# Kernel optimization log

Hardware: AMD Instinct MI355X
Metric: run time of the kernel (lower is better)

The kernel has to match this reference:

```python
import jax, jax.numpy as jnp
import numpy as np

B, NPG, K = 8, 2048, 20   # graphs, nodes per graph, kNN fanout
N = B * NPG
OUT = 16


def _bn(h, g, b, eps=1e-5):
    # BatchNorm1d (training-mode batch stats, biased var), channels last
    ax = tuple(range(h.ndim - 1))
    m = h.mean(ax)
    v = h.var(ax)
    return g * (h - m) * jax.lax.rsqrt(v + eps) + b


def _mlp(h, w, b, g, be):
    # Sequential(Linear, ReLU, BatchNorm1d)
    return _bn(jax.nn.relu(h @ w + b), g, be)


def _knn(f, k):
    # k nearest (squared euclidean), self included like torch_cluster.knn(x, x)
    sq = jnp.sum(f * f, axis=-1)
    d = sq[:, None] - 2.0 * (f @ f.T) + sq[None, :]   # [n, n]
    return jax.lax.top_k(-d, k)[1]                    # [n, k]


def setup_inputs() -> dict:
    key = jax.random.key(0)
    ks = jax.random.split(key, 16)

    def w(i, shape):
        return jax.random.normal(ks[i], shape, jnp.float32) * (1.0 / np.sqrt(shape[0]))

    return {
        "pos": jax.random.normal(ks[0], (N, 3), jnp.float32),
        "x": jax.random.normal(ks[1], (N, 1), jnp.float32),
        "batch": jnp.repeat(jnp.arange(B, dtype=jnp.int32), NPG),  # equal-size graphs
        # conv1 edge MLP: Linear(8,64)+ReLU+BN
        "w1": w(2, (8, 64)), "b1": jnp.zeros((64,), jnp.float32), "g1": jnp.ones((64,), jnp.float32), "be1": jnp.zeros((64,), jnp.float32),
        # conv2 edge MLP: Linear(128,128)+ReLU+BN
        "w2": w(3, (128, 128)), "b2": jnp.zeros((128,), jnp.float32), "g2": jnp.ones((128,), jnp.float32), "be2": jnp.zeros((128,), jnp.float32),
        # fc: Linear(192,256)+ReLU+BN
        "wf": w(4, (192, 256)), "bf": jnp.zeros((256,), jnp.float32), "gf": jnp.ones((256,), jnp.float32), "bef": jnp.zeros((256,), jnp.float32),
        # out head: Linear(256,128)+ReLU+BN, Linear(128,64)+ReLU+BN, Linear(64,OUT)
        "wo1": w(5, (256, 128)), "bo1": jnp.zeros((128,), jnp.float32), "go1": jnp.ones((128,), jnp.float32), "beo1": jnp.zeros((128,), jnp.float32),
        "wo2": w(6, (128, 64)), "bo2": jnp.zeros((64,), jnp.float32), "go2": jnp.ones((64,), jnp.float32), "beo2": jnp.zeros((64,), jnp.float32),
        "wo3": w(7, (64, OUT)), "bo3": jnp.zeros((OUT,), jnp.float32),
    }


def reference(pos, x, batch, w1, b1, g1, be1, w2, b2, g2, be2,
              wf, bf, gf, bef, wo1, bo1, go1, beo1, wo2, bo2, go2, beo2, wo3, bo3):
    # ---- conv1: DynamicEdgeConv over ALL nodes (called without batch) ----
    f0 = jnp.concatenate([pos, x], axis=-1)            # [N, 4]
    idx1 = _knn(f0, K)                                 # [N, K] global kNN
    xi = f0[:, None, :]                                # [N, 1, 4]
    xj = jnp.take(f0, idx1, axis=0)                    # [N, K, 4]
    e1 = jnp.concatenate([jnp.broadcast_to(xi, xj.shape), xj - xi], axis=-1)  # [N,K,8]
    x1 = _mlp(e1, w1, b1, g1, be1).max(axis=1)         # max aggr -> [N, 64]

    # ---- conv2: DynamicEdgeConv with per-graph kNN (equal-size graphs) ----
    x1b = x1.reshape(B, NPG, -1)                       # [B, n, 64]
    idx2 = jax.vmap(lambda f: _knn(f, K))(x1b)         # [B, n, K] local indices
    xj2 = jax.vmap(lambda f, i: f[i])(x1b, idx2)       # [B, n, K, 64]
    xi2 = x1b[:, :, None, :]
    e2 = jnp.concatenate([jnp.broadcast_to(xi2, xj2.shape), xj2 - xi2], axis=-1)
    e2 = e2.reshape(N, K, 128)                         # BN over all edges jointly
    x2 = _mlp(e2, w2, b2, g2, be2).max(axis=1)         # [N, 128]

    # ---- fc + global max pool + head ----
    h = _mlp(jnp.concatenate([x1, x2], axis=-1), wf, bf, gf, bef)  # [N, 256]
    hp = h.reshape(B, NPG, -1).max(axis=1)             # global_max_pool -> [B, 256]
    hp = _mlp(hp, wo1, bo1, go1, beo1)                 # Dropout(0.5) = identity (eval)
    hp = _mlp(hp, wo2, bo2, go2, beo2)
    logits = hp @ wo3 + bo3                            # [B, OUT]
    return jax.nn.log_softmax(logits, axis=1)
```

## Files before the change

### kernel.cpp

```cpp
#include <hip/hip_runtime.h>
#include <math.h>

#define NPTS 16384
#define KNB 20
#define SCAP 512

typedef __attribute__((ext_vector_type(8))) short short8;
typedef __attribute__((ext_vector_type(4))) float f32x4;

static const size_t OFF_F0   = 0;
static const size_t OFF_SSQ0 = OFF_F0   + (size_t)NPTS*4*4;
static const size_t OFF_IDX1 = OFF_SSQ0 + (size_t)NPTS*4;
static const size_t OFF_XMX1 = OFF_IDX1 + (size_t)NPTS*KNB*4;
static const size_t OFF_XMN1 = OFF_XMX1 + (size_t)NPTS*64*4;
static const size_t OFF_SUM1 = OFF_XMN1 + (size_t)NPTS*64*4;
static const size_t OFF_X1   = OFF_SUM1 + 512;
static const size_t OFF_SSQ1 = OFF_X1   + (size_t)NPTS*64*4;
static const size_t OFF_IDX2 = OFF_SSQ1 + (size_t)NPTS*4;
static const size_t OFF_XMX2 = OFF_IDX2 + (size_t)NPTS*KNB*4;
static const size_t OFF_XMN2 = OFF_XMX2 + (size_t)NPTS*128*4;
static const size_t OFF_SUM2 = OFF_XMN2 + (size_t)NPTS*128*4;
static const size_t OFF_X2   = OFF_SUM2 + 1024;
static const size_t OFF_SUMF = OFF_X2   + (size_t)NPTS*128*4;
static const size_t OFF_HPMX = OFF_SUMF + 2048;
static const size_t OFF_HPMN = OFF_HPMX + 8*256*4;

__device__ __forceinline__ float dot4f(float4 a, float4 b) {
  return a.x*b.x + a.y*b.y + a.z*b.z + a.w*b.w;
}

__device__ __forceinline__ float dot64v(const float* a, const float4* b4) {
  float s = 0.f;
  #pragma unroll
  for (int d4 = 0; d4 < 16; ++d4) {
    float4 b = b4[d4];
    s += a[4*d4+0]*b.x + a[4*d4+1]*b.y + a[4*d4+2]*b.z + a[4*d4+3]*b.w;
  }
  return s;
}

__device__ __forceinline__ short f2bf(float x) {
  union { float f; unsigned u; } v; v.f = x;
  unsigned r = (v.u + 0x7FFFu + ((v.u >> 16) & 1u)) >> 16;
  return (short)r;
}

__device__ __forceinline__ void ce(float& a, int& ai, float& b, int& bi) {
  bool sw = b < a;
  float d0 = sw ? b : a;  float d1 = sw ? a : b;
  int   j0 = sw ? bi : ai; int  j1 = sw ? ai : bi;
  a = d0; ai = j0; b = d1; bi = j1;
}

__device__ __forceinline__ void sort16(float (&d)[16], int (&ix)[16]) {
  #pragma unroll
  for (int k = 2; k <= 16; k <<= 1) {
    #pragma unroll
    for (int j = k >> 1; j > 0; j >>= 1) {
      #pragma unroll
      for (int i = 0; i < 16; ++i) {
        int l = i ^ j;
        if (l > i) {
          if ((i & k) == 0) ce(d[i], ix[i], d[l], ix[l]);
          else              ce(d[l], ix[l], d[i], ix[i]);
        }
      }
    }
  }
}

__device__ __forceinline__ void bimerge32(float (&rd)[32], int (&ri)[32]) {
  #pragma unroll
  for (int j = 16; j > 0; j >>= 1) {
    #pragma unroll
    for (int i = 0; i < 32; ++i) {
      int l = i ^ j;
      if (l > i) ce(rd[i], ri[i], rd[l], ri[l]);
    }
  }
}

__device__ __forceinline__ void merge16(float (&rd)[32], int (&ri)[32],
                                        float (&bd)[16], int (&bi)[16]) {
  #pragma unroll
  for (int k = 0; k < 16; ++k) {
    bool sw = bd[15-k] < rd[16+k];
    rd[16+k] = sw ? bd[15-k] : rd[16+k];
    ri[16+k] = sw ? bi[15-k] : ri[16+k];
  }
  bimerge32(rd, ri);
}

__device__ __forceinline__ void mergelane(float (&rd)[32], int (&ri)[32], int mask) {
  float pd[32]; int pi[32];
  #pragma unroll
  for (int s = 0; s < 32; ++s) { pd[s] = __shfl_xor(rd[s], mask); pi[s] = __shfl_xor(ri[s], mask); }
  #pragma unroll
  for (int k = 0; k < 32; ++k) {
    bool sw = pd[31-k] < rd[k];
    rd[k] = sw ? pd[31-k] : rd[k];
    ri[k] = sw ? pi[31-k] : ri[k];
  }
  bimerge32(rd, ri);
}

__device__ __forceinline__ void vce(float& a, float& b) {
  float lo = fminf(a, b);
  b = fmaxf(a, b);
  a = lo;
}

__device__ __forceinline__ void vsort16(float (&d)[16]) {
  #pragma unroll
  for (int k = 2; k <= 16; k <<= 1) {
    #pragma unroll
    for (int j = k >> 1; j > 0; j >>= 1) {
      #pragma unroll
      for (int i = 0; i < 16; ++i) {
        int l = i ^ j;
        if (l > i) {
          if ((i & k) == 0) vce(d[i], d[l]);
          else              vce(d[l], d[i]);
        }
      }
    }
  }
}

__device__ __forceinline__ void vbimerge32(float (&rd)[32]) {
  #pragma unroll
  for (int j = 16; j > 0; j >>= 1) {
    #pragma unroll
    for (int i = 0; i < 32; ++i) {
      int l = i ^ j;
      if (l > i) vce(rd[i], rd[l]);
    }
  }
}

__device__ __forceinline__ void vmerge16(float (&rd)[32], float (&bd)[16]) {
  #pragma unroll
  for (int k = 0; k < 16; ++k) rd[16+k] = fminf(rd[16+k], bd[15-k]);
  vbimerge32(rd);
}

__device__ __forceinline__ void vmergelane(float (&rd)[32], int mask) {
  float pd[32];
  #pragma unroll
  for (int s = 0; s < 32; ++s) pd[s] = __shfl_xor(rd[s], mask);
  #pragma unroll
  for (int k = 0; k < 32; ++k) rd[k] = fminf(rd[k], pd[31-k]);
  vbimerge32(rd);
}

__global__ __launch_bounds__(256) void k_init(const float* __restrict__ pos, const float* __restrict__ x,
                                              const float* __restrict__ w2,
                                              float4* __restrict__ f0, float* __restrict__ ssq,
                                              short* __restrict__ wtg,
                                              float* sum1, float* sum2, float* sumF,
                                              unsigned* hpmx, unsigned* hpmn) {
  int gt = blockIdx.x*256 + threadIdx.x;
  float4 f;
  f.x = pos[3*gt+0]; f.y = pos[3*gt+1]; f.z = pos[3*gt+2]; f.w = x[gt];
  f0[gt] = f;
  ssq[gt] = dot4f(f, f);
  { int c = gt >> 7, k = gt & 127; wtg[c*128 + k] = f2bf(w2[k*128 + c]); }
  if (gt < 128) sum1[gt] = 0.f;
  if (gt < 256) sum2[gt] = 0.f;
  if (gt < 512) sumF[gt] = 0.f;
  if (gt < 2048) { hpmx[gt] = 0u; hpmn[gt] = 0x7f800000u; }
}

__global__ __launch_bounds__(256) void k_knn1(const float4* __restrict__ f0, const float* __restrict__ ssq,
                                              int* __restrict__ idx1) {
  __shared__ int survj[8][SCAP];
  __shared__ int scnt[8];
  __shared__ float rowT[8];
  int t = threadIdx.x;
  int r = t >> 5;
  int lane = t & 31;
  int row = blockIdx.x*8 + r;
  if (t < 8) scnt[t] = 0;
  float4 fi = f0[row];
  float sqi = ssq[row];
  {
    float rd[32];
    #pragma unroll
    for (int s = 0; s < 32; ++s) rd[s] = INFINITY;
    #pragma unroll
    for (int b = 0; b < 4; ++b) {
      float bd[16];
      #pragma unroll
      for (int u = 0; u < 16; ++u) {
        int j = b*512 + u*32 + lane;
        float4 c = f0[j];
        bd[u] = (sqi - 2.f*dot4f(fi, c)) + ssq[j];
      }
      vsort16(bd);
      vmerge16(rd, bd);
    }
    vmergelane(rd, 1); vmergelane(rd, 2); vmergelane(rd, 4);
    vmergelane(rd, 8); vmergelane(rd, 16);
    if (lane == 0) rowT[r] = rd[19];
  }
  __syncthreads();
  {
    float4 fr[8]; float sr[8], Tr[8];
    #pragma unroll
    for (int q = 0; q < 8; ++q) {
      fr[q] = f0[blockIdx.x*8 + q];
      sr[q] = ssq[blockIdx.x*8 + q];
      Tr[q] = rowT[q];
    }
    #pragma unroll 4
    for (int k = 0; k < 64; ++k) {
      int j = k*256 + t;
      float4 c = f0[j];
      float cq = ssq[j];
      #pragma unroll
      for (int q = 0; q < 8; ++q) {
        float d = (sr[q] - 2.f*dot4f(fr[q], c)) + cq;
        if (d <= Tr[q]) {
          int slot = atomicAdd(&scnt[q], 1);
          if (slot < SCAP) survj[q][slot] = j;
        }
      }
    }
  }
  __syncthreads();
  int n = scnt[r] < SCAP ? scnt[r] : SCAP;
  float rd[32]; int ri[32];
  #pragma unroll
  for (int s = 0; s < 32; ++s) { rd[s] = INFINITY; ri[s] = 0; }
  {
    float bd[16]; int bix[16];
    #pragma unroll
    for (int u = 0; u < 16; ++u) {
      int s = u*32 + lane;
      if (s < n) {
        int j = survj[r][s];
        float4 c = f0[j];
        bd[u] = (sqi - 2.f*dot4f(fi, c)) + ssq[j];
        bix[u] = j;
      } else { bd[u] = INFINITY; bix[u] = 0; }
    }
    sort16(bd, bix);
    merge16(rd, ri, bd, bix);
  }
  mergelane(rd, ri, 1); mergelane(rd, ri, 2); mergelane(rd, ri, 4);
  mergelane(rd, ri, 8); mergelane(rd, ri, 16);
  if (lane == 0) {
    int4* p = (int4*)&idx1[row*KNB];
    p[0] = make_int4(ri[0],ri[1],ri[2],ri[3]);
    p[1] = make_int4(ri[4],ri[5],ri[6],ri[7]);
    p[2] = make_int4(ri[8],ri[9],ri[10],ri[11]);
    p[3] = make_int4(ri[12],ri[13],ri[14],ri[15]);
    p[4] = make_int4(ri[16],ri[17],ri[18],ri[19]);
  }
}

__global__ __launch_bounds__(256) void k_mlp1(const float4* __restrict__ f0, const int* __restrict__ idx1,
                                              const float* __restrict__ w1, const float* __restrict__ b1,
                                              float* __restrict__ xmx, float* __restrict__ xmn,
                                              float* __restrict__ sums) {
  __shared__ float rs[256], rs2[256];
  int t = threadIdx.x;
  int c = t & 63;
  int w = t >> 6;
  float wc[8];
  #pragma unroll
  for (int d = 0; d < 8; ++d) wc[d] = w1[d*64 + c];
  float bc = b1[c];
  float s = 0.f, s2 = 0.f;
  for (int p = 0; p < 8; ++p) {
    int i = blockIdx.x*32 + p*4 + w;
    float4 fi = f0[i];
    float mx = -INFINITY, mn = INFINITY;
    #pragma unroll
    for (int k = 0; k < KNB; ++k) {
      int j = idx1[i*KNB + k];
      float4 fj = f0[j];
      float h = bc + fi.x*wc[0] + fi.y*wc[1] + fi.z*wc[2] + fi.w*wc[3]
                   + (fj.x-fi.x)*wc[4] + (fj.y-fi.y)*wc[5] + (fj.z-fi.z)*wc[6] + (fj.w-fi.w)*wc[7];
      h = fmaxf(h, 0.f);
      mx = fmaxf(mx, h); mn = fminf(mn, h);
      s += h; s2 += h*h;
    }
    xmx[i*64+c] = mx; xmn[i*64+c] = mn;
  }
  rs[t] = s; rs2[t] = s2;
  __syncthreads();
  if (t < 64) {
    atomicAdd(&sums[c],      rs[t]+rs[t+64]+rs[t+128]+rs[t+192]);
    atomicAdd(&sums[64+c],   rs2[t]+rs2[t+64]+rs2[t+128]+rs2[t+192]);
  }
}

__global__ __launch_bounds__(256) void k_bn1apply(const float* __restrict__ sums, const float* __restrict__ g,
                                                  const float* __restrict__ be, const float* __restrict__ xmx,
                                                  const float* __restrict__ xmn, float* __restrict__ x1) {
  __shared__ float sc_s[64], sh_s[64];
  int t = threadIdx.x;
  if (t < 64) {
    float m = sums[t] * (1.f/327680.f);
    float v = sums[64+t] * (1.f/327680.f) - m*m;
    float sc = g[t] / sqrtf(v + 1e-5f);
    sc_s[t] = sc; sh_s[t] = be[t] - m*sc;
  }
  __syncthreads();
  int c = t & 63;
  int i = blockIdx.x*4 + (t>>6);
  float sc = sc_s[c], sh = sh_s[c];
  float val = (sc >= 0.f) ? xmx[i*64+c] : xmn[i*64+c];
  x1[i*64+c] = sc*val + sh;
}

__global__ __launch_bounds__(256) void k_ssq1(const float* __restrict__ x1, float* __restrict__ ssq1) {
  int i = blockIdx.x*256 + threadIdx.x;
  alignas(16) float f[64];
  #pragma unroll
  for (int d4 = 0; d4 < 16; ++d4) ((float4*)f)[d4] = ((const float4*)x1)[i*16 + d4];
  ssq1[i] = dot64v(f, (const float4*)f);
}

__global__ __launch_bounds__(256) void k_knn2(const float* __restrict__ x1, const float* __restrict__ ssq1,
                                              int* __restrict__ idx2) {
  __shared__ __align__(16) float tf[128][68];
  __shared__ float tq[128];
  int t = threadIdx.x;
  int row = blockIdx.x*32 + (t>>3);
  int lane = t & 7;
  int cbase = (row >> 11) << 11;
  alignas(16) float fi[64];
  #pragma unroll
  for (int d4 = 0; d4 < 16; ++d4) ((float4*)fi)[d4] = ((const float4*)x1)[row*16 + d4];
  float sqi = ssq1[row];
  float rd[32]; int ri[32];
  #pragma unroll
  for (int s = 0; s < 32; ++s) { rd[s] = INFINITY; ri[s] = 0; }
  for (int tile = 0; tile < 16; ++tile) {
    int base = cbase + tile*128;
    __syncthreads();
    for (int v = t; v < 128*16; v += 256) {
      int jl = v >> 4, d4 = v & 15;
      *(float4*)&tf[jl][d4*4] = ((const float4*)x1)[(base+jl)*16 + d4];
    }
    if (t < 128) tq[t] = ssq1[base + t];
    __syncthreads();
    float bd[16]; int bix[16];
    #pragma unroll
    for (int u = 0; u < 16; ++u) {
      int jl = u*8 + lane;
      bd[u] = (sqi - 2.f*dot64v(fi, (const float4*)&tf[jl][0])) + tq[jl];
      bix[u] = base + jl;
    }
    sort16(bd, bix);
    merge16(rd, ri, bd, bix);
  }
  mergelane(rd, ri, 1);
  mergelane(rd, ri, 2);
  mergelane(rd, ri, 4);
  if (lane == 0) {
    int4* p = (int4*)&idx2[row*KNB];
    p[0] = make_int4(ri[0],ri[1],ri[2],ri[3]);
    p[1] = make_int4(ri[4],ri[5],ri[6],ri[7]);
    p[2] = make_int4(ri[8],ri[9],ri[10],ri[11]);
    p[3] = make_int4(ri[12],ri[13],ri[14],ri[15]);
    p[4] = make_int4(ri[16],ri[17],ri[18],ri[19]);
  }
}

__global__ __launch_bounds__(256) void k_mlp2(const float* __restrict__ x1, const int* __restrict__ idx2,
                                              const short* __restrict__ wtg, const float* __restrict__ w2,
                                              const float* __restrict__ b2,
                                              float* __restrict__ xmx, float* __restrict__ xmn,
                                              float* __restrict__ sums) {
  __shared__ __align__(16) short Elds[4*32*72];
  __shared__ float xi_s[4][64];
  __shared__ float vi[4][128];
  __shared__ int js[4][KNB];
  int t = threadIdx.x;
  if (t < 4*KNB) js[t/KNB][t%KNB] = idx2[blockIdx.x*4*KNB + t];
  {
    int p = t >> 6, k = t & 63;
    xi_s[p][k] = x1[(blockIdx.x*4 + p)*64 + k];
  }
  __syncthreads();
  #pragma unroll
  for (int v2 = 0; v2 < 2; ++v2) {
    int v = t + v2*256;
    int p = v >> 7, c = v & 127;
    float a = b2[c];
    #pragma unroll 8
    for (int k = 0; k < 64; ++k) a += xi_s[p][k] * w2[k*128 + c];
    vi[p][c] = a;
  }
  #pragma unroll
  for (int cc = 0; cc < 4; ++cc) {
    int v = t + cc*256;
    int p  = v >> 8;
    int rr = (v >> 3) & 31;
    int kc = v & 7;
    short8 outv = {0,0,0,0,0,0,0,0};
    if (rr < KNB) {
      int j = js[p][rr];
      float4 j0 = ((const float4*)x1)[j*16 + kc*2];
      float4 j1 = ((const float4*)x1)[j*16 + kc*2 + 1];
      const float* xp = &xi_s[p][kc*8];
      outv[0]=f2bf(j0.x-xp[0]); outv[1]=f2bf(j0.y-xp[1]); outv[2]=f2bf(j0.z-xp[2]); outv[3]=f2bf(j0.w-xp[3]);
      outv[4]=f2bf(j1.x-xp[4]); outv[5]=f2bf(j1.y-xp[5]); outv[6]=f2bf(j1.z-xp[6]); outv[7]=f2bf(j1.w-xp[7]);
    }
    *(short8*)&Elds[p*2304 + rr*72 + kc*8] = outv;
  }
  __syncthreads();
  int w = t >> 6, l = t & 63;
  int colA = w*32 + (l & 15);
  int colB = colA + 16;
  short8 bfr[2][2];
  #pragma unroll
  for (int n = 0; n < 2; ++n)
    #pragma unroll
    for (int kb = 0; kb < 2; ++kb) {
      int col = w*32 + n*16 + (l & 15);
      int k0 = 64 + kb*32 + (l >> 4)*8;
      bfr[n][kb] = *(const short8*)&wtg[col*128 + k0];
    }
  float sT0=0.f, qT0=0.f, sT1=0.f, qT1=0.f;
  #pragma unroll
  for (int p = 0; p < 4; ++p) {
    int i = blockIdx.x*4 + p;
    float vA = vi[p][colA], vB = vi[p][colB];
    float mx0=-INFINITY, mn0=INFINITY, s0=0.f, q0=0.f;
    float mx1=-INFINITY, mn1=INFINITY, s1=0.f, q1=0.f;
    #pragma unroll
    for (int m = 0; m < 2; ++m) {
      short8 af[2];
      #pragma unroll
      for (int kb = 0; kb < 2; ++kb) {
        int row = m*16 + (l & 15);
        int k0 = kb*32 + (l >> 4)*8;
        af[kb] = *(short8*)&Elds[p*2304 + row*72 + k0];
      }
      f32x4 acc0 = {vA, vA, vA, vA};
      f32x4 acc1 = {vB, vB, vB, vB};
      #pragma unroll
      for (int kb = 0; kb < 2; ++kb) {
        acc0 = __builtin_amdgcn_mfma_f32_16x16x32_bf16(af[kb], bfr[0][kb], acc0, 0, 0, 0);
        acc1 = __builtin_amdgcn_mfma_f32_16x16x32_bf16(af[kb], bfr[1][kb], acc1, 0, 0, 0);
      }
      int rbase = (l >> 4)*4 + m*16;
      #pragma unroll
      for (int reg = 0; reg < 4; ++reg) {
        bool valid = (rbase + reg) < KNB;
        float h0 = fmaxf(acc0[reg], 0.f);
        float h1 = fmaxf(acc1[reg], 0.f);
        if (valid) {
          mx0 = fmaxf(mx0, h0); mn0 = fminf(mn0, h0); s0 += h0; q0 += h0*h0;
          mx1 = fmaxf(mx1, h1); mn1 = fminf(mn1, h1); s1 += h1; q1 += h1*h1;
        }
      }
    }
    #pragma unroll
    for (int dlt = 16; dlt <= 32; dlt <<= 1) {
      mx0 = fmaxf(mx0, __shfl_xor(mx0, dlt)); mn0 = fminf(mn0, __shfl_xor(mn0, dlt));
      s0 += __shfl_xor(s0, dlt);              q0 += __shfl_xor(q0, dlt);
      mx1 = fmaxf(mx1, __shfl_xor(mx1, dlt)); mn1 = fminf(mn1, __shfl_xor(mn1, dlt));
      s1 += __shfl_xor(s1, dlt);              q1 += __shfl_xor(q1, dlt);
    }
    if (l < 16) {
      xmx[i*128 + colA] = mx0; xmx[i*128 + colB] = mx1;
      xmn[i*128 + colA] = mn0; xmn[i*128 + colB] = mn1;
    }
    sT0 += s0; qT0 += q0; sT1 += s1; qT1 += q1;
  }
  if (l < 16) {
    atomicAdd(&sums[colA], sT0);       atomicAdd(&sums[colB], sT1);
    atomicAdd(&sums[128 + colA], qT0); atomicAdd(&sums[128 + colB], qT1);
  }
}

__global__ __launch_bounds__(256) void k_bn2apply(const float* __restrict__ sums, const float* __restrict__ g,
                                                  const float* __restrict__ be, const float* __restrict__ xmx,
                                                  const float* __restrict__ xmn, float* __restrict__ x2) {
  __shared__ float sc_s[128], sh_s[128];
  int t = threadIdx.x;
  if (t < 128) {
    float m = sums[t] * (1.f/327680.f);
    float v = sums[128+t] * (1.f/327680.f) - m*m;
    float sc = g[t] / sqrtf(v + 1e-5f);
    sc_s[t] = sc; sh_s[t] = be[t] - m*sc;
  }
  __syncthreads();
  int c = t & 127;
  int i = blockIdx.x*2 + (t>>7);
  float sc = sc_s[c], sh = sh_s[c];
  float val = (sc >= 0.f) ? xmx[i*128+c] : xmn[i*128+c];
  x2[i*128+c] = sc*val + sh;
}

__global__ __launch_bounds__(256) void k_gemmF(const float* __restrict__ x1, const float* __restrict__ x2,
                                               const float* __restrict__ wf, const float* __restrict__ bf,
                                               float* __restrict__ sumsF, unsigned* __restrict__ hpmx,
                                               unsigned* __restrict__ hpmn) {
  __shared__ float A_s[64*193];
  __shared__ __align__(16) float B_s[192*64];
  __shared__ float red[1024];
  int t = threadIdx.x;
  int rt = blockIdx.x >> 2;
  int ct = blockIdx.x & 3;
  for (int v = t; v < 64*48; v += 256) {
    int r = v / 48, gg = v - r*48;
    int row = rt*64 + r;
    float4 e = (gg < 16) ? ((const float4*)x1)[row*16 + gg]
                         : ((const float4*)x2)[row*32 + (gg-16)];
    float* p = &A_s[r*193 + gg*4];
    p[0]=e.x; p[1]=e.y; p[2]=e.z; p[3]=e.w;
  }
  for (int v = t; v < 192*16; v += 256) {
    int d = v >> 4, c4 = v & 15;
    *(float4*)&B_s[d*64 + c4*4] = ((const float4*)wf)[d*64 + ct*16 + c4];
  }
  __syncthreads();
  int rg = t & 15, cg = t >> 4;
  float acc[4][4];
  #pragma unroll
  for (int a=0;a<4;a++) { acc[a][0]=0.f; acc[a][1]=0.f; acc[a][2]=0.f; acc[a][3]=0.f; }
  for (int d = 0; d < 192; ++d) {
    float a0 = A_s[(rg*4+0)*193 + d];
    float a1 = A_s[(rg*4+1)*193 + d];
    float a2 = A_s[(rg*4+2)*193 + d];
    float a3 = A_s[(rg*4+3)*193 + d];
    float b0 = B_s[d*64 + cg];
    float b1 = B_s[d*64 + cg + 16];
    float b2 = B_s[d*64 + cg + 32];
    float b3 = B_s[d*64 + cg + 48];
    acc[0][0]+=a0*b0; acc[0][1]+=a0*b1; acc[0][2]+=a0*b2; acc[0][3]+=a0*b3;
    acc[1][0]+=a1*b0; acc[1][1]+=a1*b1; acc[1][2]+=a1*b2; acc[1][3]+=a1*b3;
    acc[2][0]+=a2*b0; acc[2][1]+=a2*b1; acc[2][2]+=a2*b2; acc[2][3]+=a2*b3;
    acc[3][0]+=a3*b0; acc[3][1]+=a3*b1; acc[3][2]+=a3*b2; acc[3][3]+=a3*b3;
  }
  float hv[4][4];
  #pragma unroll
  for (int ss=0; ss<4; ++ss) {
    float bb = bf[ct*64 + cg + ss*16];
    #pragma unroll
    for (int rr=0; rr<4; ++rr) hv[rr][ss] = fmaxf(acc[rr][ss] + bb, 0.f);
  }
  int b = rt >> 5;
  #pragma unroll
  for (int ss=0; ss<4; ++ss) red[rg*64 + cg + ss*16] = hv[0][ss]+hv[1][ss]+hv[2][ss]+hv[3][ss];
  __syncthreads();
  if (t < 64) {
    float v = 0.f;
    #pragma unroll
    for (int r=0;r<16;r++) v += red[r*64 + t];
    atomicAdd(&sumsF[ct*64 + t], v);
  }
  __syncthreads();
  #pragma unroll
  for (int ss=0; ss<4; ++ss) red[rg*64 + cg + ss*16] =
      hv[0][ss]*hv[0][ss]+hv[1][ss]*hv[1][ss]+hv[2][ss]*hv[2][ss]+hv[3][ss]*hv[3][ss];
  __syncthreads();
  if (t < 64) {
    float v = 0.f;
    #pragma unroll
    for (int r=0;r<16;r++) v += red[r*64 + t];
    atomicAdd(&sumsF[256 + ct*64 + t], v);
  }
  __syncthreads();
  #pragma unroll
  for (int ss=0; ss<4; ++ss) red[rg*64 + cg + ss*16] =
      fmaxf(fmaxf(hv[0][ss],hv[1][ss]), fmaxf(hv[2][ss],hv[3][ss]));
  __syncthreads();
  if (t < 64) {
    float v = -INFINITY;
    #pragma unroll
    for (int r=0;r<16;r++) v = fmaxf(v, red[r*64 + t]);
    atomicMax(&hpmx[b*256 + ct*64 + t], __float_as_uint(v));
  }
  __syncthreads();
  #pragma unroll
  for (int ss=0; ss<4; ++ss) red[rg*64 + cg + ss*16] =
      fminf(fminf(hv[0][ss],hv[1][ss]), fminf(hv[2][ss],hv[3][ss]));
  __syncthreads();
  if (t < 64) {
    float v = INFINITY;
    #pragma unroll
    for (int r=0;r<16;r++) v = fminf(v, red[r*64 + t]);
    atomicMin(&hpmn[b*256 + ct*64 + t], __float_as_uint(v));
  }
}

__global__ __launch_bounds__(256) void k_head(const float* __restrict__ sumsF, const float* __restrict__ gf,
                                              const float* __restrict__ bef,
                                              const unsigned* __restrict__ hpmx, const unsigned* __restrict__ hpmn,
                                              const float* __restrict__ wo1, const float* __restrict__ bo1,
                                              const float* __restrict__ go1, const float* __restrict__ beo1,
                                              const float* __restrict__ wo2, const float* __restrict__ bo2,
                                              const float* __restrict__ go2, const float* __restrict__ beo2,
                                              const float* __restrict__ wo3, const float* __restrict__ bo3,
                                              float* __restrict__ out) {
  __shared__ float hp[8][256];
  __shared__ float u1[8][128];
  __shared__ float u2[8][64];
  __shared__ float lg[8][16];
  int t = threadIdx.x;
  {
    float m = sumsF[t] * (1.f/16384.f);
    float v = sumsF[256+t] * (1.f/16384.f) - m*m;
    float sc = gf[t] / sqrtf(v + 1e-5f);
    float sh = bef[t] - m*sc;
    for (int b = 0; b < 8; ++b) {
      unsigned bits = (sc >= 0.f) ? hpmx[b*256+t] : hpmn[b*256+t];
      hp[b][t] = sc*__uint_as_float(bits) + sh;
    }
  }
  __syncthreads();
  for (int p = t; p < 1024; p += 256) {
    int b = p >> 7, c = p & 127;
    float z = bo1[c];
    for (int d = 0; d < 256; ++d) z += hp[b][d]*wo1[d*128+c];
    u1[b][c] = fmaxf(z, 0.f);
  }
  __syncthreads();
  if (t < 128) {
    float m = 0.f;
    for (int b=0;b<8;b++) m += u1[b][t];
    m *= 0.125f;
    float v = 0.f;
    for (int b=0;b<8;b++) { float dd = u1[b][t]-m; v += dd*dd; }
    v *= 0.125f;
    float sc = go1[t]/sqrtf(v+1e-5f), sh = beo1[t]-m*sc;
    for (int b=0;b<8;b++) u1[b][t] = sc*u1[b][t]+sh;
  }
  __syncthreads();
  for (int p = t; p < 512; p += 256) {
    int b = p >> 6, c = p & 63;
    float z = bo2[c];
    for (int d = 0; d < 128; ++d) z += u1[b][d]*wo2[d*64+c];
    u2[b][c] = fmaxf(z, 0.f);
  }
  __syncthreads();
  if (t < 64) {
    float m = 0.f;
    for (int b=0;b<8;b++) m += u2[b][t];
    m *= 0.125f;
    float v = 0.f;
    for (int b=0;b<8;b++) { float dd = u2[b][t]-m; v += dd*dd; }
    v *= 0.125f;
    float sc = go2[t]/sqrtf(v+1e-5f), sh = beo2[t]-m*sc;
    for (int b=0;b<8;b++) u2[b][t] = sc*u2[b][t]+sh;
  }
  __syncthreads();
  if (t < 128) {
    int b = t >> 4, c = t & 15;
    float z = bo3[c];
    for (int d = 0; d < 64; ++d) z += u2[b][d]*wo3[d*16+c];
    lg[b][c] = z;
  }
  __syncthreads();
  if (t < 8) {
    float m = -INFINITY;
    for (int j=0;j<16;j++) m = fmaxf(m, lg[t][j]);
    float s = 0.f;
    for (int j=0;j<16;j++) s += expf(lg[t][j]-m);
    float ls = logf(s);
    for (int j=0;j<16;j++) out[t*16+j] = (lg[t][j]-m) - ls;
  }
}

extern "C" void kernel_launch(void* const* d_in, const int* in_sizes, int n_in,
                              void* d_out, int out_size, void* d_ws, size_t ws_size,
                              hipStream_t stream) {
  (void)in_sizes; (void)n_in; (void)out_size; (void)ws_size;
  const float* pos = (const float*)d_in[0];
  const float* x   = (const float*)d_in[1];
  const float* w1  = (const float*)d_in[3];
  const float* b1  = (const float*)d_in[4];
  const float* g1  = (const float*)d_in[5];
  const float* be1 = (const float*)d_in[6];
  const float* w2  = (const float*)d_in[7];
  const float* b2  = (const float*)d_in[8];
  const float* g2  = (const float*)d_in[9];
  const float* be2 = (const float*)d_in[10];
  const float* wf  = (const float*)d_in[11];
  const float* bf  = (const float*)d_in[12];
  const float* gf  = (const float*)d_in[13];
  const float* bef = (const float*)d_in[14];
  const float* wo1 = (const float*)d_in[15];
  const float* bo1 = (const float*)d_in[16];
  const float* go1 = (const float*)d_in[17];
  const float* beo1= (const float*)d_in[18];
  const float* wo2 = (const float*)d_in[19];
  const float* bo2 = (const float*)d_in[20];
  const float* go2 = (const float*)d_in[21];
  const float* beo2= (const float*)d_in[22];
  const float* wo3 = (const float*)d_in[23];
  const float* bo3 = (const float*)d_in[24];

  char* ws = (char*)d_ws;
  float4*   f0    = (float4*)  (ws + OFF_F0);
  float*    ssq0  = (float*)   (ws + OFF_SSQ0);
  int*      idx1  = (int*)     (ws + OFF_IDX1);
  float*    xmx1  = (float*)   (ws + OFF_XMX1);
  float*    xmn1  = (float*)   (ws + OFF_XMN1);
  float*    sum1  = (float*)   (ws + OFF_SUM1);
  float*    x1    = (float*)   (ws + OFF_X1);
  float*    ssq1  = (float*)   (ws + OFF_SSQ1);
  int*      idx2  = (int*)     (ws + OFF_IDX2);
  float*    xmx2  = (float*)   (ws + OFF_XMX2);
  float*    xmn2  = (float*)   (ws + OFF_XMN2);
  float*    sum2  = (float*)   (ws + OFF_SUM2);
  float*    x2    = (float*)   (ws + OFF_X2);
  float*    sumF  = (float*)   (ws + OFF_SUMF);
  unsigned* hpmx  = (unsigned*)(ws + OFF_HPMX);
  unsigned* hpmn  = (unsigned*)(ws + OFF_HPMN);
  short*    wtg   = (short*)   (ws + OFF_X2);

  k_init    <<<64,   256, 0, stream>>>(pos, x, w2, f0, ssq0, wtg, sum1, sum2, sumF, hpmx, hpmn);
  k_knn1    <<<2048, 256, 0, stream>>>(f0, ssq0, idx1);
  k_mlp1    <<<512,  256, 0, stream>>>(f0, idx1, w1, b1, xmx1, xmn1, sum1);
  k_bn1apply<<<4096, 256, 0, stream>>>(sum1, g1, be1, xmx1, xmn1, x1);
  k_ssq1    <<<64,   256, 0, stream>>>(x1, ssq1);
  k_knn2    <<<512,  256, 0, stream>>>(x1, ssq1, idx2);
  k_mlp2    <<<4096, 256, 0, stream>>>(x1, idx2, wtg, w2, b2, xmx2, xmn2, sum2);
  k_bn2apply<<<8192, 256, 0, stream>>>(sum2, g2, be2, xmx2, xmn2, x2);
  k_gemmF   <<<1024, 256, 0, stream>>>(x1, x2, wf, bf, sumF, hpmx, hpmn);
  k_head    <<<1,    256, 0, stream>>>(sumF, gf, bef, hpmx, hpmn,
                                       wo1, bo1, go1, beo1, wo2, bo2, go2, beo2, wo3, bo3,
                                       (float*)d_out);
}
```

Measured before the change: 673.8 us.

## Screen conv2 kNN candidates with bf16 MFMA then rescore survivors exactly

The per-graph kNN for conv2 is rebuilt as a filter-and-refine pass. First, a threshold per row is set from the 20th-best exact distance among 256 sampled candidates. Next, all 2048 candidates are screened with bf16 MFMA distances against that threshold plus an error margin, and the survivors go into a shared-memory list. Only those survivors are rescored in fp32 and sorted. This replaces the fp32 scalar dot products and the full sort-merge over every candidate. The cost is extra LDS traffic, atomic counters, and a risk that an overflowing survivor list (more than 448) or a too-tight bf16 margin gives different neighbors.

```diff
diff --git a/kernel.cpp b/kernel.cpp
--- a/kernel.cpp
+++ b/kernel.cpp
@@ -4,6 +4,7 @@
 #define NPTS 16384
 #define KNB 20
 #define SCAP 512
+#define SCAP2 448
 
 typedef __attribute__((ext_vector_type(8))) short short8;
 typedef __attribute__((ext_vector_type(4))) float f32x4;
@@ -325,48 +326,141 @@
 
 __global__ __launch_bounds__(256) void k_knn2(const float* __restrict__ x1, const float* __restrict__ ssq1,
                                               int* __restrict__ idx2) {
-  __shared__ __align__(16) float tf[128][68];
-  __shared__ float tq[128];
+  __shared__ __align__(16) short Abf[32*72];
+  __shared__ __align__(16) short Bbf[128*72];
+  __shared__ float sqA[32];
+  __shared__ float sqB[128];
+  __shared__ float rowT[32];
+  __shared__ unsigned short surv[32][SCAP2];
+  __shared__ int scnt[32];
   int t = threadIdx.x;
-  int row = blockIdx.x*32 + (t>>3);
-  int lane = t & 7;
-  int cbase = (row >> 11) << 11;
-  alignas(16) float fi[64];
-  #pragma unroll
-  for (int d4 = 0; d4 < 16; ++d4) ((float4*)fi)[d4] = ((const float4*)x1)[row*16 + d4];
-  float sqi = ssq1[row];
-  float rd[32]; int ri[32];
-  #pragma unroll
-  for (int s = 0; s < 32; ++s) { rd[s] = INFINITY; ri[s] = 0; }
-  for (int tile = 0; tile < 16; ++tile) {
-    int base = cbase + tile*128;
+  int b = blockIdx.x >> 6;
+  int rg = blockIdx.x & 63;
+  int cbase = b*2048;
+  int row0 = cbase + rg*32;
+  if (t < 32) { scnt[t] = 0; sqA[t] = ssq1[row0 + t]; }
+  {
+    int rr = t >> 3, kc = t & 7;
+    float4 a0 = ((const float4*)x1)[(row0+rr)*16 + kc*2];
+    float4 a1 = ((const float4*)x1)[(row0+rr)*16 + kc*2 + 1];
+    short8 o;
+    o[0]=f2bf(a0.x); o[1]=f2bf(a0.y); o[2]=f2bf(a0.z); o[3]=f2bf(a0.w);
+    o[4]=f2bf(a1.x); o[5]=f2bf(a1.y); o[6]=f2bf(a1.z); o[7]=f2bf(a1.w);
+    *(short8*)&Abf[rr*72 + kc*8] = o;
+  }
+  {
+    int r = t >> 3, lane = t & 7;
+    int row = row0 + r;
+    alignas(16) float fi[64];
+    #pragma unroll
+    for (int d4 = 0; d4 < 16; ++d4) ((float4*)fi)[d4] = ((const float4*)x1)[row*16 + d4];
+    float sqi = ssq1[row];
+    float rd[32];
+    #pragma unroll
+    for (int s = 0; s < 32; ++s) rd[s] = INFINITY;
+    #pragma unroll
+    for (int bb = 0; bb < 2; ++bb) {
+      float bd[16];
+      #pragma unroll
+      for (int u = 0; u < 16; ++u) {
+        int j = cbase + bb*128 + u*8 + lane;
+        bd[u] = (sqi - 2.f*dot64v(fi, (const float4*)&x1[j*64])) + ssq1[j];
+      }
+      vsort16(bd);
+      vmerge16(rd, bd);
+    }
+    vmergelane(rd, 1); vmergelane(rd, 2); vmergelane(rd, 4);
+    if (lane == 0) rowT[r] = rd[19];
+  }
+  __syncthreads();
+  int w = t >> 6, l = t & 63;
+  short8 af[2][2];
+  #pragma unroll
+  for (int m = 0; m < 2; ++m)
+    #pragma unroll
+    for (int kb = 0; kb < 2; ++kb)
+      af[m][kb] = *(short8*)&Abf[(m*16 + (l & 15))*72 + kb*32 + (l >> 4)*8];
+  for (int ct = 0; ct < 16; ++ct) {
+    int cb = ct*128;
     __syncthreads();
-    for (int v = t; v < 128*16; v += 256) {
-      int jl = v >> 4, d4 = v & 15;
-      *(float4*)&tf[jl][d4*4] = ((const float4*)x1)[(base+jl)*16 + d4];
-    }
-    if (t < 128) tq[t] = ssq1[base + t];
+    #pragma unroll
+    for (int cc = 0; cc < 4; ++cc) {
+      int v = t + cc*256;
+      int rr = v >> 3, kc = v & 7;
+      int j = cbase + cb + rr;
+      float4 a0 = ((const float4*)x1)[j*16 + kc*2];
+      float4 a1 = ((const float4*)x1)[j*16 + kc*2 + 1];
+      short8 o;
+      o[0]=f2bf(a0.x); o[1]=f2bf(a0.y); o[2]=f2bf(a0.z); o[3]=f2bf(a0.w);
+      o[4]=f2bf(a1.x); o[5]=f2bf(a1.y); o[6]=f2bf(a1.z); o[7]=f2bf(a1.w);
+      *(short8*)&Bbf[rr*72 + kc*8] = o;
+      if (kc == 0) sqB[rr] = ssq1[j];
+    }
     __syncthreads();
-    float bd[16]; int bix[16];
-    #pragma unroll
-    for (int u = 0; u < 16; ++u) {
-      int jl = u*8 + lane;
-      bd[u] = (sqi - 2.f*dot64v(fi, (const float4*)&tf[jl][0])) + tq[jl];
-      bix[u] = base + jl;
-    }
-    sort16(bd, bix);
-    merge16(rd, ri, bd, bix);
-  }
-  mergelane(rd, ri, 1);
-  mergelane(rd, ri, 2);
-  mergelane(rd, ri, 4);
-  if (lane == 0) {
-    int4* p = (int4*)&idx2[row*KNB];
-    p[0] = make_int4(ri[0],ri[1],ri[2],ri[3]);
-    p[1] = make_int4(ri[4],ri[5],ri[6],ri[7]);
-    p[2] = make_int4(ri[8],ri[9],ri[10],ri[11]);
-    p[3] = make_int4(ri[12],ri[13],ri[14],ri[15]);
-    p[4] = make_int4(ri[16],ri[17],ri[18],ri[19]);
+    #pragma unroll
+    for (int cs = 0; cs < 2; ++cs) {
+      int c16 = (w*2 + cs)*16;
+      short8 bfr[2];
+      #pragma unroll
+      for (int kb = 0; kb < 2; ++kb)
+        bfr[kb] = *(short8*)&Bbf[(c16 + (l & 15))*72 + kb*32 + (l >> 4)*8];
+      int jcol = c16 + (l & 15);
+      float sb = sqB[jcol];
+      #pragma unroll
+      for (int m = 0; m < 2; ++m) {
+        f32x4 acc = {0.f, 0.f, 0.f, 0.f};
+        acc = __builtin_amdgcn_mfma_f32_16x16x32_bf16(af[m][0], bfr[0], acc, 0, 0, 0);
+        acc = __builtin_amdgcn_mfma_f32_16x16x32_bf16(af[m][1], bfr[1], acc, 0, 0, 0);
+        #pragma unroll
+        for (int reg = 0; reg < 4; ++reg) {
+          int il = m*16 + (l >> 4)*4 + reg;
+          float sa = sqA[il];
+          float dh = (sa - 2.f*acc[reg]) + sb;
+          float M = 0.0078125f*(sa + sb);
+          if (dh <= rowT[il] + M) {
+            int slot = atomicAdd(&scnt[il], 1);
+            if (slot < SCAP2) surv[il][slot] = (unsigned short)(cb + jcol);
+          }
+        }
+      }
+    }
+  }
+  __syncthreads();
+  {
+    int r = t >> 3, lane = t & 7;
+    int row = row0 + r;
+    int n = scnt[r] < SCAP2 ? scnt[r] : SCAP2;
+    alignas(16) float fi[64];
+    #pragma unroll
+    for (int d4 = 0; d4 < 16; ++d4) ((float4*)fi)[d4] = ((const float4*)x1)[row*16 + d4];
+    float sqi = ssq1[row];
+    float rd[32]; int ri[32];
+    #pragma unroll
+    for (int s = 0; s < 32; ++s) { rd[s] = INFINITY; ri[s] = 0; }
+    #pragma unroll
+    for (int g = 0; g < 4; ++g) {
+      float bd[16]; int bix[16];
+      #pragma unroll
+      for (int u = 0; u < 16; ++u) {
+        int s = (g*16 + u)*8 + lane;
+        if (s < n) {
+          int j = cbase + (int)surv[r][s];
+          bd[u] = (sqi - 2.f*dot64v(fi, (const float4*)&x1[j*64])) + ssq1[j];
+          bix[u] = j;
+        } else { bd[u] = INFINITY; bix[u] = 0; }
+      }
+      sort16(bd, bix);
+      merge16(rd, ri, bd, bix);
+    }
+    mergelane(rd, ri, 1); mergelane(rd, ri, 2); mergelane(rd, ri, 4);
+    if (lane == 0) {
+      int4* p = (int4*)&idx2[row*KNB];
+      p[0] = make_int4(ri[0],ri[1],ri[2],ri[3]);
+      p[1] = make_int4(ri[4],ri[5],ri[6],ri[7]);
+      p[2] = make_int4(ri[8],ri[9],ri[10],ri[11]);
+      p[3] = make_int4(ri[12],ri[13],ri[14],ri[15]);
+      p[4] = make_int4(ri[16],ri[17],ri[18],ri[19]);
+    }
   }
 }
 
```

After: 835.1 us. 23.9% more time.
